# Kernel optimization log

Measured on AMD Instinct MI355X. Metric: run time of the kernel, lower is better.

Reference implementation:

```python
import jax, jax.numpy as jnp
import numpy as np

TAU_PLUS = 0.02
TAU_MINUS = 0.02
TAU_X = 0.101
A_TRIPLET = 0.0065
HOMEOSTATIC_RATE = 0.1
DT = 0.001
SPIKE_P = 0.05  # spike probability used to binarize inputs


def setup_inputs() -> dict:
    key = jax.random.key(0)
    k1, k2, k3 = jax.random.split(key, 3)
    B, P, Q, T = 16, 2048, 2048, 256
    pre_spikes = (jax.random.uniform(k1, (B, P, T)) < SPIKE_P).astype(jnp.float32)
    post_spikes = (jax.random.uniform(k2, (B, Q, T)) < SPIKE_P).astype(jnp.float32)
    weights = jax.random.normal(k3, (P, Q), dtype=jnp.float32) * 0.1
    meta_A_plus = jnp.float32(0.01)
    meta_A_minus = jnp.float32(0.012)
    return {"pre_spikes": pre_spikes, "post_spikes": post_spikes,
            "weights": weights, "meta_A_plus": meta_A_plus,
            "meta_A_minus": meta_A_minus}


def _traces(spikes_tbn, decay):
    """Trace value used at step t: x_t = decay * (x_{t-1} + s_{t-1}), x_0 = 0."""
    def step(carry, s):
        x = decay * carry          # decayed trace, used for this step's update
        return x + s, x            # spike added AFTER the update, per original
    init = jnp.zeros(spikes_tbn.shape[1:], spikes_tbn.dtype)
    _, xs = jax.lax.scan(step, init, spikes_tbn)
    return xs  # [T, B, N]


def reference(pre_spikes, post_spikes, weights, meta_A_plus, meta_A_minus):
    B, P, T = pre_spikes.shape
    exp_plus = jnp.exp(jnp.float32(-DT / TAU_PLUS))
    exp_minus = jnp.exp(jnp.float32(-DT / TAU_MINUS))
    exp_x = jnp.exp(jnp.float32(-DT / TAU_X))

    pre_t = jnp.transpose(pre_spikes, (2, 0, 1))    # [T, B, P]
    post_t = jnp.transpose(post_spikes, (2, 0, 1))  # [T, B, Q]

    x_pre = _traces(pre_t, exp_plus)     # [T, B, P]
    x_post = _traces(post_t, exp_minus)  # [T, B, Q]
    x_trip = _traces(post_t, exp_x)      # [T, B, Q]

    # Per-step outer products summed over time == one big contraction over (t, b).
    ltp = jnp.einsum('tbp,tbq->pq', x_pre, post_t) * meta_A_plus
    triplet = jnp.einsum('tbp,tbq->pq', x_pre, post_t * x_trip) * A_TRIPLET
    ltd = jnp.einsum('tbp,tbq->pq', pre_t, x_post) * meta_A_minus
    weight_updates = ltp + triplet - ltd

    # Homeostatic scaling (fresh module: activity history holds only this sample)
    current_activity = (pre_spikes.sum() + post_spikes.sum()) / (B * T)
    scaling_factor = jnp.sqrt(HOMEOSTATIC_RATE / (current_activity + 1e-6))

    updated_weights = weights + weight_updates * scaling_factor
    return jnp.clip(updated_weights, -2.0, 2.0)
```

## Files before the change

kernel.cpp:

```cpp
#include <hip/hip_runtime.h>


constexpr int TB = 16;
constexpr int NP = 2048;
constexpr int NQ = 2048;
constexpr int TT = 256;
constexpr int KH = TB * TT;
constexpr int KT = 2 * KH;

typedef unsigned short ushort_t;
typedef __attribute__((ext_vector_type(8))) __bf16 bf16x8;
typedef __attribute__((ext_vector_type(4))) float f32x4;

__device__ __forceinline__ unsigned bf1(float f) {
    unsigned u = __builtin_bit_cast(unsigned, f);
    return (u + 0x7FFFu + ((u >> 16) & 1u)) >> 16;
}
__device__ __forceinline__ unsigned pack2(float lo, float hi) {
    return bf1(lo) | (bf1(hi) << 16);
}
__device__ __forceinline__ unsigned spk2(float a, float b) {
    return ((a != 0.f) ? 0x3F80u : 0u) | ((b != 0.f) ? 0x3F800000u : 0u);
}

constexpr float DF1 = 0.95122942450071400910f;
constexpr float DF2 = DF1 * DF1;
constexpr float DF4 = DF2 * DF2;
constexpr float DF8 = DF4 * DF4;
constexpr float DF16 = DF8 * DF8;
constexpr float DF32 = DF16 * DF16;
constexpr float DF64 = DF32 * DF32;

constexpr float DX1 = 0.99014786386058731819f;
constexpr float DX2 = DX1 * DX1;
constexpr float DX4 = DX2 * DX2;
constexpr float DX8 = DX4 * DX4;
constexpr float DX16 = DX8 * DX8;
constexpr float DX32 = DX16 * DX16;
constexpr float DX64 = DX32 * DX32;

template <int K>
__device__ __forceinline__ float seg_step(float b, float pw, int sl) {
    float t = __shfl_up(b, K, 64);
    return (sl >= K) ? fmaf(pw, t, b) : b;
}
__device__ __forceinline__ float scan16(float c, float p1, float p2, float p4,
                                        float p8, int sl) {
    c = seg_step<1>(c, p1, sl);
    c = seg_step<2>(c, p2, sl);
    c = seg_step<4>(c, p4, sl);
    c = seg_step<8>(c, p8, sl);
    return c;
}
__device__ __forceinline__ float fold4(float4 u, float d) {
    float C = d * u.x;
    C = d * (C + u.y); C = d * (C + u.z); C = d * (C + u.w);
    return C;
}
__device__ __forceinline__ float4 expand4(float x, float4 u, float d) {
    float4 t;
    t.x = x; x = d * (x + u.x);
    t.y = x; x = d * (x + u.y);
    t.z = x; x = d * (x + u.z);
    t.w = x;
    return t;
}

__global__ __launch_bounds__(256) void stage_traces(
    const float* __restrict__ pre, const float* __restrict__ post,
    const float* __restrict__ mApP, const float* __restrict__ mAmP,
    ushort_t* __restrict__ Ab, ushort_t* __restrict__ Bb,
    float* __restrict__ partials)
{
    const int tid  = threadIdx.x;
    const int lane = tid & 63;
    const int wv   = tid >> 6;
    const int sl   = lane & 15;
    const int rowg = blockIdx.x * 16 + wv * 4 + (lane >> 4);
    const bool isPre = rowg < TB * NP;
    const int m = isPre ? rowg : rowg - TB * NP;
    const int b = m >> 11;
    const int r = m & 2047;

    const float4* srcRow = (const float4*)((isPre ? pre : post) + (size_t)m * TT);
    const float4 u0 = srcRow[sl];
    const float4 u1 = srcRow[16 + sl];
    const float4 u2 = srcRow[32 + sl];
    const float4 u3 = srcRow[48 + sl];

    float cnt = ((u0.x + u0.y) + (u0.z + u0.w)) + ((u1.x + u1.y) + (u1.z + u1.w))
              + ((u2.x + u2.y) + (u2.z + u2.w)) + ((u3.x + u3.y) + (u3.z + u3.w));

    const int hi = lane | 15;

    float bf0 = scan16(fold4(u0, DF1), DF4, DF8, DF16, DF32, sl);
    float bf1_ = scan16(fold4(u1, DF1), DF4, DF8, DF16, DF32, sl);
    float bf2 = scan16(fold4(u2, DF1), DF4, DF8, DF16, DF32, sl);
    float bf3 = scan16(fold4(u3, DF1), DF4, DF8, DF16, DF32, sl);
    const float Tf0 = __shfl(bf0, hi, 64);
    const float Tf1 = __shfl(bf1_, hi, 64);
    const float Tf2 = __shfl(bf2, hi, 64);
    const float Xf1 = Tf0;
    const float Xf2 = fmaf(DF64, Xf1, Tf1);
    const float Xf3 = fmaf(DF64, Xf2, Tf2);
    float ef0 = __shfl_up(bf0, 1, 64);
    float ef1 = __shfl_up(bf1_, 1, 64);
    float ef2 = __shfl_up(bf2, 1, 64);
    float ef3 = __shfl_up(bf3, 1, 64);
    if (sl == 0) { ef0 = 0.f; ef1 = 0.f; ef2 = 0.f; ef3 = 0.f; }
    float pf = 1.f;
    if (sl & 1) pf *= DF4;
    if (sl & 2) pf *= DF8;
    if (sl & 4) pf *= DF16;
    if (sl & 8) pf *= DF32;
    const float4 t0 = expand4(ef0,                 u0, DF1);
    const float4 t1 = expand4(fmaf(pf, Xf1, ef1),  u1, DF1);
    const float4 t2 = expand4(fmaf(pf, Xf2, ef2),  u2, DF1);
    const float4 t3 = expand4(fmaf(pf, Xf3, ef3),  u3, DF1);

    ushort_t* oA = (isPre ? Ab : Bb) + (size_t)r * KT + b * TT + 4 * sl;

    if (isPre) {
        *(uint2*)(oA)            = uint2{pack2(t0.x, t0.y), pack2(t0.z, t0.w)};
        *(uint2*)(oA + 64)       = uint2{pack2(t1.x, t1.y), pack2(t1.z, t1.w)};
        *(uint2*)(oA + 128)      = uint2{pack2(t2.x, t2.y), pack2(t2.z, t2.w)};
        *(uint2*)(oA + 192)      = uint2{pack2(t3.x, t3.y), pack2(t3.z, t3.w)};
        *(uint2*)(oA + KH)       = uint2{spk2(u0.x, u0.y), spk2(u0.z, u0.w)};
        *(uint2*)(oA + KH + 64)  = uint2{spk2(u1.x, u1.y), spk2(u1.z, u1.w)};
        *(uint2*)(oA + KH + 128) = uint2{spk2(u2.x, u2.y), spk2(u2.z, u2.w)};
        *(uint2*)(oA + KH + 192) = uint2{spk2(u3.x, u3.y), spk2(u3.z, u3.w)};
    } else {
        float bx0 = scan16(fold4(u0, DX1), DX4, DX8, DX16, DX32, sl);
        float bx1 = scan16(fold4(u1, DX1), DX4, DX8, DX16, DX32, sl);
        float bx2 = scan16(fold4(u2, DX1), DX4, DX8, DX16, DX32, sl);
        float bx3 = scan16(fold4(u3, DX1), DX4, DX8, DX16, DX32, sl);
        const float Tx0 = __shfl(bx0, hi, 64);
        const float Tx1 = __shfl(bx1, hi, 64);
        const float Tx2 = __shfl(bx2, hi, 64);
        const float Xx1 = Tx0;
        const float Xx2 = fmaf(DX64, Xx1, Tx1);
        const float Xx3 = fmaf(DX64, Xx2, Tx2);
        float ex0 = __shfl_up(bx0, 1, 64);
        float ex1 = __shfl_up(bx1, 1, 64);
        float ex2 = __shfl_up(bx2, 1, 64);
        float ex3 = __shfl_up(bx3, 1, 64);
        if (sl == 0) { ex0 = 0.f; ex1 = 0.f; ex2 = 0.f; ex3 = 0.f; }
        float px = 1.f;
        if (sl & 1) px *= DX4;
        if (sl & 2) px *= DX8;
        if (sl & 4) px *= DX16;
        if (sl & 8) px *= DX32;
        const float4 w0 = expand4(ex0,                u0, DX1);
        const float4 w1 = expand4(fmaf(px, Xx1, ex1), u1, DX1);
        const float4 w2 = expand4(fmaf(px, Xx2, ex2), u2, DX1);
        const float4 w3 = expand4(fmaf(px, Xx3, ex3), u3, DX1);

        const float Ap = *mApP;
        const float Am = *mAmP;
        auto av2 = [&](float sa, float ta, float sb, float tb) -> unsigned {
            unsigned lo = (sa != 0.f) ? bf1(fmaf(0.0065f, ta, Ap)) : 0u;
            unsigned hi2 = (sb != 0.f) ? bf1(fmaf(0.0065f, tb, Ap)) : 0u;
            return lo | (hi2 << 16);
        };
        *(uint2*)(oA)       = uint2{av2(u0.x, w0.x, u0.y, w0.y), av2(u0.z, w0.z, u0.w, w0.w)};
        *(uint2*)(oA + 64)  = uint2{av2(u1.x, w1.x, u1.y, w1.y), av2(u1.z, w1.z, u1.w, w1.w)};
        *(uint2*)(oA + 128) = uint2{av2(u2.x, w2.x, u2.y, w2.y), av2(u2.z, w2.z, u2.w, w2.w)};
        *(uint2*)(oA + 192) = uint2{av2(u3.x, w3.x, u3.y, w3.y), av2(u3.z, w3.z, u3.w, w3.w)};
        *(uint2*)(oA + KH)       = uint2{pack2(-Am * t0.x, -Am * t0.y), pack2(-Am * t0.z, -Am * t0.w)};
        *(uint2*)(oA + KH + 64)  = uint2{pack2(-Am * t1.x, -Am * t1.y), pack2(-Am * t1.z, -Am * t1.w)};
        *(uint2*)(oA + KH + 128) = uint2{pack2(-Am * t2.x, -Am * t2.y), pack2(-Am * t2.z, -Am * t2.w)};
        *(uint2*)(oA + KH + 192) = uint2{pack2(-Am * t3.x, -Am * t3.y), pack2(-Am * t3.z, -Am * t3.w)};
    }

    #pragma unroll
    for (int off = 32; off > 0; off >>= 1)
        cnt += __shfl_down(cnt, off, 64);
    __shared__ float wsum[4];
    if (lane == 0) wsum[wv] = cnt;
    __syncthreads();
    if (tid == 0)
        partials[blockIdx.x] = (wsum[0] + wsum[1]) + (wsum[2] + wsum[3]);
}

__device__ __forceinline__ void async16(const ushort_t* g, ushort_t* l) {
    __builtin_amdgcn_global_load_lds(
        (const __attribute__((address_space(1))) unsigned int*)g,
        (__attribute__((address_space(3))) unsigned int*)l,
        16, 0, 0);
}

#define FENCE() asm volatile("" ::: "memory")
#define BAR()   do { FENCE(); __builtin_amdgcn_s_barrier(); FENCE(); } while (0)
#define LGKM0() asm volatile("s_waitcnt lgkmcnt(0)" ::: "memory")
#define VMC8()  asm volatile("s_waitcnt vmcnt(8)" ::: "memory")
#define VMC0()  asm volatile("s_waitcnt vmcnt(0)" ::: "memory")

#define STAGE(GP, LP, KI, H) do {                                           \
    const ushort_t* _g = (GP) + (size_t)(H) * 128 * KT + (size_t)(KI) * 64; \
    ushort_t* _l = (LP) + (H) * 8192;                                       \
    async16(_g + ofG,  _l + ld0);                                           \
    async16(_g + ofG2, _l + ld1);                                           \
} while (0)

#define RD_A(BUF, QM) do {                                                  \
    _Pragma("unroll")                                                       \
    for (int mi = 0; mi < 4; ++mi) {                                        \
        const ushort_t* _r = &As[BUF][(QM) * 8192 + aBase + mi * 1024];     \
        af[mi][0] = *(const bf16x8*)(_r + sK0);                             \
        af[mi][1] = *(const bf16x8*)(_r + sK1);                             \
    }                                                                       \
} while (0)

#define RD_B(BUF, QN, BV) do {                                              \
    _Pragma("unroll")                                                       \
    for (int ni = 0; ni < 2; ++ni) {                                        \
        const ushort_t* _r = &Bs[BUF][(QN) * 8192 + bBase + ni * 1024];     \
        BV[ni][0] = *(const bf16x8*)(_r + sK0);                             \
        BV[ni][1] = *(const bf16x8*)(_r + sK1);                             \
    }                                                                       \
} while (0)

#define MFMAQ(QM, QN, BV) do {                                              \
    __builtin_amdgcn_s_setprio(1);                                          \
    _Pragma("unroll")                                                       \
    for (int ks = 0; ks < 2; ++ks)                                          \
        _Pragma("unroll")                                                   \
        for (int mi = 0; mi < 4; ++mi)                                      \
            _Pragma("unroll")                                               \
            for (int ni = 0; ni < 2; ++ni)                                  \
                acc[(QM)*4+mi][(QN)*2+ni] =                                 \
                    __builtin_amdgcn_mfma_f32_16x16x32_bf16(                \
                        af[mi][ks], BV[ni][ks],                             \
                        acc[(QM)*4+mi][(QN)*2+ni], 0, 0, 0);                \
    __builtin_amdgcn_s_setprio(0);                                          \
} while (0)

__global__ __launch_bounds__(512) void gemm8(
    const ushort_t* __restrict__ Ab, const ushort_t* __restrict__ Bb,
    const float* __restrict__ sp, float* __restrict__ scaleBuf,
    float* __restrict__ P0, float* __restrict__ P1,
    float* __restrict__ P2, float* __restrict__ P3)
{
    __shared__ ushort_t As[2][256 * 64];
    __shared__ ushort_t Bs[2][256 * 64];
    __shared__ float red[8];

    const int tid  = threadIdx.x;
    const int lane = tid & 63;
    const int wv   = tid >> 6;
    const int wr   = wv >> 2;
    const int wc   = wv & 3;
    const int quad = lane >> 4;
    const int m16  = lane & 15;

    if (blockIdx.x == 0) {
        float v = 0.f;
        #pragma unroll
        for (int i = 0; i < 8; ++i) v += sp[tid + i * 512];
        #pragma unroll
        for (int off = 32; off > 0; off >>= 1)
            v += __shfl_down(v, off, 64);
        if (lane == 0) red[wv] = v;
        __syncthreads();
        if (tid == 0) {
            float s = ((red[0] + red[1]) + (red[2] + red[3]))
                    + ((red[4] + red[5]) + (red[6] + red[7]));
            scaleBuf[0] = sqrtf(0.1f / (s * (1.0f / 4096.0f) + 1e-6f));
        }
    }

    const int id  = blockIdx.x;
    const int xcd = id & 7;
    const int j   = id >> 3;
    const int z   = j & 3;
    const int t   = j >> 2;
    const int pt  = ((xcd >> 1) << 1) | (t >> 2);
    const int qt  = ((xcd & 1) << 2) | (t & 3);
    const int p0  = pt * 256;
    const int q0  = qt * 256;
    const int kbase = z * (KT / 4);

    const ushort_t* Agp = Ab + (size_t)p0 * KT + kbase;
    const ushort_t* Bgp = Bb + (size_t)q0 * KT + kbase;
    const int rIn  = tid >> 3;
    const int rIn2 = rIn + 64;
    const size_t ofG  = (size_t)rIn  * KT + (size_t)((((tid & 7) ^ (rIn  & 7))) * 8);
    const size_t ofG2 = (size_t)rIn2 * KT + (size_t)((((tid & 7) ^ (rIn2 & 7))) * 8);
    const int ld0 = tid * 8;
    const int ld1 = 4096 + tid * 8;

    const int x8  = (m16 & 7) * 8;
    const int sK0 = (quad * 8) ^ x8;
    const int sK1 = ((quad + 4) * 8) ^ x8;
    const int aBase = (wr * 64 + m16) * 64;
    const int bBase = (wc * 32 + m16) * 64;

    f32x4 acc[8][4] = {};
    bf16x8 af[4][2], bv0[2][2], bv1[2][2];

    STAGE(Agp, As[0], 0, 0);
    STAGE(Agp, As[0], 0, 1);
    STAGE(Bgp, Bs[0], 0, 0);
    STAGE(Bgp, Bs[0], 0, 1);
    STAGE(Agp, As[1], 1, 0);
    STAGE(Agp, As[1], 1, 1);
    STAGE(Bgp, Bs[1], 1, 0);
    STAGE(Bgp, Bs[1], 1, 1);
    VMC8();
    BAR();

    #pragma unroll 1
    for (int it = 0; it < 16; ++it) {
        const int k2 = 2 * it;
        const bool pf = (it < 15);
        RD_A(0, 0);
        RD_B(0, 0, bv0);
        BAR(); LGKM0();
        MFMAQ(0, 0, bv0);
        BAR();
        RD_B(0, 1, bv1);
        if (pf) { STAGE(Agp, As[0], k2 + 2, 0); STAGE(Bgp, Bs[0], k2 + 2, 0); }
        BAR(); LGKM0();
        MFMAQ(0, 1, bv1);
        BAR();
        RD_A(0, 1);
        if (pf) STAGE(Bgp, Bs[0], k2 + 2, 1);
        BAR(); LGKM0();
        MFMAQ(1, 1, bv1);
        BAR();
        if (pf) STAGE(Agp, As[0], k2 + 2, 1);
        BAR();
        MFMAQ(1, 0, bv0);
        if (pf) { VMC8(); } else { VMC0(); }
        BAR();
        RD_A(1, 0);
        RD_B(1, 0, bv0);
        BAR(); LGKM0();
        MFMAQ(0, 0, bv0);
        BAR();
        RD_B(1, 1, bv1);
        if (pf) { STAGE(Agp, As[1], k2 + 3, 0); STAGE(Bgp, Bs[1], k2 + 3, 0); }
        BAR(); LGKM0();
        MFMAQ(0, 1, bv1);
        BAR();
        RD_A(1, 1);
        if (pf) STAGE(Bgp, Bs[1], k2 + 3, 1);
        BAR(); LGKM0();
        MFMAQ(1, 1, bv1);
        BAR();
        if (pf) STAGE(Agp, As[1], k2 + 3, 1);
        BAR();
        MFMAQ(1, 0, bv0);
        if (pf) { VMC8(); }
        BAR();
    }

    float* P = (z == 0) ? P0 : ((z == 1) ? P1 : ((z == 2) ? P2 : P3));
    #pragma unroll
    for (int m = 0; m < 8; ++m) {
        const int prow = p0 + ((m >> 2) << 7) + wr * 64 + (m & 3) * 16 + quad * 4;
        #pragma unroll
        for (int n = 0; n < 4; ++n) {
            const int qcol = q0 + ((n >> 1) << 7) + wc * 32 + (n & 1) * 16 + m16;
            #pragma unroll
            for (int r = 0; r < 4; ++r)
                P[(size_t)(prow + r) * NQ + qcol] = acc[m][n][r];
        }
    }
}

__global__ __launch_bounds__(256, 2) void gemm_split(
    const ushort_t* __restrict__ Ab, const ushort_t* __restrict__ Bb,
    const float* __restrict__ sp, float* __restrict__ scaleBuf,
    float* __restrict__ P0, float* __restrict__ P1)
{
    __shared__ ushort_t Ls[2][128 * 64];
    __shared__ ushort_t Rs[2][128 * 64];
    __shared__ float red[4];

    const int tid  = threadIdx.x;
    const int lane = tid & 63;
    const int wv   = tid >> 6;
    const int wr   = wv >> 1;
    const int wc   = wv & 1;
    const int quad = lane >> 4;
    const int m16  = lane & 15;

    if (blockIdx.x == 0) {
        float v = 0.f;
        #pragma unroll
        for (int i = 0; i < 16; ++i) v += sp[tid + i * 256];
        #pragma unroll
        for (int off = 32; off > 0; off >>= 1)
            v += __shfl_down(v, off, 64);
        if (lane == 0) red[wv] = v;
        __syncthreads();
        if (tid == 0) {
            float s = (red[0] + red[1]) + (red[2] + red[3]);
            scaleBuf[0] = sqrtf(0.1f / (s * (1.0f / 4096.0f) + 1e-6f));
        }
    }

    const int id  = blockIdx.x;
    const int xcd = id & 7;
    const int j5  = id >> 3;
    const int z   = j5 & 1;
    const int t   = j5 >> 1;
    const int pt  = ((xcd >> 1) << 2) + (t >> 3);
    const int qt  = ((xcd & 1) << 3) + (t & 7);

    const int p0 = pt * 128;
    const int q0 = qt * 128;
    const int kbase = z * (KT / 2);
    const int ldsbase = wv * 512;

    const ushort_t* gaP[4];
    const ushort_t* gbP[4];
    #pragma unroll
    for (int rr = 0; rr < 4; ++rr) {
        const int c   = rr * 256 + tid;
        const int row = c >> 3;
        const int kk8 = (c & 7) ^ (row & 7);
        gaP[rr] = Ab + (size_t)(p0 + row) * KT + kbase + kk8 * 8;
        gbP[rr] = Bb + (size_t)(q0 + row) * KT + kbase + kk8 * 8;
    }

    f32x4 acc[4][4] = {};

    auto stageF = [&](int buf) {
        #pragma unroll
        for (int rr = 0; rr < 4; ++rr) {
            async16(gaP[rr], &Ls[buf][rr * 2048 + ldsbase]);
            async16(gbP[rr], &Rs[buf][rr * 2048 + ldsbase]);
            gaP[rr] += 64;
            gbP[rr] += 64;
        }
    };
    auto computeF = [&](int buf) {
        #pragma unroll
        for (int ks = 0; ks < 2; ++ks) {
            bf16x8 afl[4], bfr[4];
            #pragma unroll
            for (int i = 0; i < 4; ++i) {
                const int row  = wr * 64 + i * 16 + m16;
                const int slot = (ks * 4 + quad) ^ (row & 7);
                afl[i] = *(const bf16x8*)&Ls[buf][row * 64 + slot * 8];
            }
            #pragma unroll
            for (int jj = 0; jj < 4; ++jj) {
                const int row  = wc * 64 + jj * 16 + m16;
                const int slot = (ks * 4 + quad) ^ (row & 7);
                bfr[jj] = *(const bf16x8*)&Rs[buf][row * 64 + slot * 8];
            }
            #pragma unroll
            for (int i = 0; i < 4; ++i)
                #pragma unroll
                for (int jj = 0; jj < 4; ++jj)
                    acc[i][jj] = __builtin_amdgcn_mfma_f32_16x16x32_bf16(
                        afl[i], bfr[jj], acc[i][jj], 0, 0, 0);
        }
    };

    constexpr int NIT = (KT / 2) / 64;
    stageF(0);
    for (int kt2 = 0; kt2 < NIT / 2; ++kt2) {
        __syncthreads();
        stageF(1);
        computeF(0);
        __syncthreads();
        if (kt2 + 1 < NIT / 2)
            stageF(0);
        computeF(1);
    }

    float* P = z ? P1 : P0;
    #pragma unroll
    for (int i = 0; i < 4; ++i) {
        const int prow = p0 + wr * 64 + i * 16 + quad * 4;
        #pragma unroll
        for (int jj = 0; jj < 4; ++jj) {
            const int qcol = q0 + wc * 64 + jj * 16 + m16;
            #pragma unroll
            for (int r2 = 0; r2 < 4; ++r2)
                P[(size_t)(prow + r2) * NQ + qcol] = acc[i][jj][r2];
        }
    }
}

__global__ __launch_bounds__(256) void merge_out4(
    const float* __restrict__ W, const float* __restrict__ P1,
    const float* __restrict__ P2, const float* __restrict__ P3,
    const float* __restrict__ scaleBuf, float* __restrict__ Out)
{
    const float scale = scaleBuf[0];
    const size_t i4 = (size_t)blockIdx.x * 256 + threadIdx.x;
    float4 w = ((const float4*)W)[i4];
    float4 a = ((const float4*)Out)[i4];
    float4 b = ((const float4*)P1)[i4];
    float4 c = ((const float4*)P2)[i4];
    float4 d = ((const float4*)P3)[i4];
    float4 o;
    o.x = fminf(fmaxf(fmaf(scale, (a.x + b.x) + (c.x + d.x), w.x), -2.f), 2.f);
    o.y = fminf(fmaxf(fmaf(scale, (a.y + b.y) + (c.y + d.y), w.y), -2.f), 2.f);
    o.z = fminf(fmaxf(fmaf(scale, (a.z + b.z) + (c.z + d.z), w.z), -2.f), 2.f);
    o.w = fminf(fmaxf(fmaf(scale, (a.w + b.w) + (c.w + d.w), w.w), -2.f), 2.f);
    ((float4*)Out)[i4] = o;
}

__global__ __launch_bounds__(256) void merge_out2(
    const float* __restrict__ W, const float* __restrict__ P1,
    const float* __restrict__ scaleBuf, float* __restrict__ Out)
{
    const float scale = scaleBuf[0];
    const size_t i4 = (size_t)blockIdx.x * 256 + threadIdx.x;
    float4 w = ((const float4*)W)[i4];
    float4 a = ((const float4*)Out)[i4];
    float4 c = ((const float4*)P1)[i4];
    float4 o;
    o.x = fminf(fmaxf(fmaf(scale, a.x + c.x, w.x), -2.f), 2.f);
    o.y = fminf(fmaxf(fmaf(scale, a.y + c.y, w.y), -2.f), 2.f);
    o.z = fminf(fmaxf(fmaf(scale, a.z + c.z, w.z), -2.f), 2.f);
    o.w = fminf(fmaxf(fmaf(scale, a.w + c.w, w.w), -2.f), 2.f);
    ((float4*)Out)[i4] = o;
}

extern "C" void kernel_launch(void* const* d_in, const int* in_sizes, int n_in,
                              void* d_out, int out_size, void* d_ws, size_t ws_size,
                              hipStream_t stream) {
    const float* pre  = (const float*)d_in[0];
    const float* post = (const float*)d_in[1];
    const float* W    = (const float*)d_in[2];
    const float* mAp  = (const float*)d_in[3];
    const float* mAm  = (const float*)d_in[4];
    float* out = (float*)d_out;

    const size_t AB = (size_t)NP * KT * 2;
    const size_t PB = (size_t)NP * NQ * 4;

    char* ws = (char*)d_ws;
    float* partials = (float*)ws;
    float* scaleBuf = (float*)(ws + 16384);
    ushort_t* Ab = (ushort_t*)(ws + 32768);
    ushort_t* Bb = (ushort_t*)(ws + 32768 + AB);
    float* P1 = (float*)(ws + 32768 + 2 * AB);
    float* P2 = (float*)(ws + 32768 + 2 * AB + PB);
    float* P3 = (float*)(ws + 32768 + 2 * AB + 2 * PB);

    stage_traces<<<dim3((TB * NP + TB * NQ) / 16), dim3(256), 0, stream>>>(
        pre, post, mAp, mAm, Ab, Bb, partials);

    if (ws_size >= 32768 + 2 * AB + 3 * PB) {
        gemm8<<<dim3(256), dim3(512), 0, stream>>>(
            Ab, Bb, partials, scaleBuf, out, P1, P2, P3);
        merge_out4<<<dim3(NP * NQ / 1024), dim3(256), 0, stream>>>(
            W, P1, P2, P3, scaleBuf, out);
    } else {
        gemm_split<<<dim3(512), dim3(256), 0, stream>>>(
            Ab, Bb, partials, scaleBuf, out, P1);
        merge_out2<<<dim3(NP * NQ / 1024), dim3(256), 0, stream>>>(
            W, P1, scaleBuf, out);
    }
}
```

Measured before the change: 200.1 us.

## Fuse split-K reduction and epilogue into GEMM via last-arriver atomic ticket

Removes the separate merge_out4 kernel by having each GEMM block take an atomic ticket per output tile after writing its split-K partial. The fourth block to finish reads the other three partials, computes the homeostatic scale itself from the stage partials, and writes the clipped final weights. This saves a kernel launch and one full pass over the output buffers, but the merge now runs on only a quarter of the blocks at the tail of the GEMM. The ticket counters are reset inside stage_traces, and the scalar reduction is repeated in every finishing block.

```diff
diff --git a/kernel.cpp b/kernel.cpp
--- a/kernel.cpp
+++ b/kernel.cpp
@@ -70,9 +70,11 @@
     const float* __restrict__ pre, const float* __restrict__ post,
     const float* __restrict__ mApP, const float* __restrict__ mAmP,
     ushort_t* __restrict__ Ab, ushort_t* __restrict__ Bb,
-    float* __restrict__ partials)
+    float* __restrict__ partials, int* __restrict__ cnt)
 {
     const int tid  = threadIdx.x;
+    if (blockIdx.x == 0 && tid < 64) cnt[tid] = 0;
+
     const int lane = tid & 63;
     const int wv   = tid >> 6;
     const int sl   = lane & 15;
@@ -88,8 +90,8 @@
     const float4 u2 = srcRow[32 + sl];
     const float4 u3 = srcRow[48 + sl];
 
-    float cnt = ((u0.x + u0.y) + (u0.z + u0.w)) + ((u1.x + u1.y) + (u1.z + u1.w))
-              + ((u2.x + u2.y) + (u2.z + u2.w)) + ((u3.x + u3.y) + (u3.z + u3.w));
+    float cnt_s = ((u0.x + u0.y) + (u0.z + u0.w)) + ((u1.x + u1.y) + (u1.z + u1.w))
+                + ((u2.x + u2.y) + (u2.z + u2.w)) + ((u3.x + u3.y) + (u3.z + u3.w));
 
     const int hi = lane | 15;
 
@@ -174,9 +176,9 @@
 
     #pragma unroll
     for (int off = 32; off > 0; off >>= 1)
-        cnt += __shfl_down(cnt, off, 64);
+        cnt_s += __shfl_down(cnt_s, off, 64);
     __shared__ float wsum[4];
-    if (lane == 0) wsum[wv] = cnt;
+    if (lane == 0) wsum[wv] = cnt_s;
     __syncthreads();
     if (tid == 0)
         partials[blockIdx.x] = (wsum[0] + wsum[1]) + (wsum[2] + wsum[3]);
@@ -235,15 +237,17 @@
     __builtin_amdgcn_s_setprio(0);                                          \
 } while (0)
 
-__global__ __launch_bounds__(512) void gemm8(
+__global__ __launch_bounds__(512) void gemm8f(
     const ushort_t* __restrict__ Ab, const ushort_t* __restrict__ Bb,
-    const float* __restrict__ sp, float* __restrict__ scaleBuf,
-    float* __restrict__ P0, float* __restrict__ P1,
-    float* __restrict__ P2, float* __restrict__ P3)
+    const float* __restrict__ sp, const float* __restrict__ W,
+    float* __restrict__ P0out, float* __restrict__ P1,
+    float* __restrict__ P2, float* __restrict__ P3,
+    int* __restrict__ cnt)
 {
     __shared__ ushort_t As[2][256 * 64];
     __shared__ ushort_t Bs[2][256 * 64];
     __shared__ float red[8];
+    __shared__ int ticket_s;
 
     const int tid  = threadIdx.x;
     const int lane = tid & 63;
@@ -252,22 +256,6 @@
     const int wc   = wv & 3;
     const int quad = lane >> 4;
     const int m16  = lane & 15;
-
-    if (blockIdx.x == 0) {
-        float v = 0.f;
-        #pragma unroll
-        for (int i = 0; i < 8; ++i) v += sp[tid + i * 512];
-        #pragma unroll
-        for (int off = 32; off > 0; off >>= 1)
-            v += __shfl_down(v, off, 64);
-        if (lane == 0) red[wv] = v;
-        __syncthreads();
-        if (tid == 0) {
-            float s = ((red[0] + red[1]) + (red[2] + red[3]))
-                    + ((red[4] + red[5]) + (red[6] + red[7]));
-            scaleBuf[0] = sqrtf(0.1f / (s * (1.0f / 4096.0f) + 1e-6f));
-        }
-    }
 
     const int id  = blockIdx.x;
     const int xcd = id & 7;
@@ -355,7 +343,7 @@
         BAR();
     }
 
-    float* P = (z == 0) ? P0 : ((z == 1) ? P1 : ((z == 2) ? P2 : P3));
+    float* P = (z == 0) ? P0out : ((z == 1) ? P1 : ((z == 2) ? P2 : P3));
     #pragma unroll
     for (int m = 0; m < 8; ++m) {
         const int prow = p0 + ((m >> 2) << 7) + wr * 64 + (m & 3) * 16 + quad * 4;
@@ -365,6 +353,44 @@
             #pragma unroll
             for (int r = 0; r < 4; ++r)
                 P[(size_t)(prow + r) * NQ + qcol] = acc[m][n][r];
+        }
+    }
+    __threadfence();
+    if (tid == 0) ticket_s = atomicAdd(&cnt[pt * 8 + qt], 1);
+    __syncthreads();
+    if (ticket_s != 3) return;
+    __threadfence();
+
+    float v = 0.f;
+    #pragma unroll
+    for (int i = 0; i < 8; ++i) v += sp[tid + i * 512];
+    #pragma unroll
+    for (int off = 32; off > 0; off >>= 1)
+        v += __shfl_down(v, off, 64);
+    if (lane == 0) red[wv] = v;
+    __syncthreads();
+    const float s = ((red[0] + red[1]) + (red[2] + red[3]))
+                  + ((red[4] + red[5]) + (red[6] + red[7]));
+    const float scale = sqrtf(0.1f / (s * (1.0f / 4096.0f) + 1e-6f));
+
+    const float* Pa; const float* Pb; const float* Pc;
+    if (z == 0)      { Pa = P1;    Pb = P2; Pc = P3; }
+    else if (z == 1) { Pa = P0out; Pb = P2; Pc = P3; }
+    else if (z == 2) { Pa = P0out; Pb = P1; Pc = P3; }
+    else             { Pa = P0out; Pb = P1; Pc = P2; }
+
+    #pragma unroll
+    for (int m = 0; m < 8; ++m) {
+        const int prow = p0 + ((m >> 2) << 7) + wr * 64 + (m & 3) * 16 + quad * 4;
+        #pragma unroll
+        for (int n = 0; n < 4; ++n) {
+            const int qcol = q0 + ((n >> 1) << 7) + wc * 32 + (n & 1) * 16 + m16;
+            #pragma unroll
+            for (int r = 0; r < 4; ++r) {
+                const size_t idx = (size_t)(prow + r) * NQ + qcol;
+                const float sum = acc[m][n][r] + ((Pa[idx] + Pb[idx]) + Pc[idx]);
+                P0out[idx] = fminf(fmaxf(fmaf(scale, sum, W[idx]), -2.f), 2.f);
+            }
         }
     }
 }
@@ -487,26 +513,6 @@
     }
 }
 
-__global__ __launch_bounds__(256) void merge_out4(
-    const float* __restrict__ W, const float* __restrict__ P1,
-    const float* __restrict__ P2, const float* __restrict__ P3,
-    const float* __restrict__ scaleBuf, float* __restrict__ Out)
-{
-    const float scale = scaleBuf[0];
-    const size_t i4 = (size_t)blockIdx.x * 256 + threadIdx.x;
-    float4 w = ((const float4*)W)[i4];
-    float4 a = ((const float4*)Out)[i4];
-    float4 b = ((const float4*)P1)[i4];
-    float4 c = ((const float4*)P2)[i4];
-    float4 d = ((const float4*)P3)[i4];
-    float4 o;
-    o.x = fminf(fmaxf(fmaf(scale, (a.x + b.x) + (c.x + d.x), w.x), -2.f), 2.f);
-    o.y = fminf(fmaxf(fmaf(scale, (a.y + b.y) + (c.y + d.y), w.y), -2.f), 2.f);
-    o.z = fminf(fmaxf(fmaf(scale, (a.z + b.z) + (c.z + d.z), w.z), -2.f), 2.f);
-    o.w = fminf(fmaxf(fmaf(scale, (a.w + b.w) + (c.w + d.w), w.w), -2.f), 2.f);
-    ((float4*)Out)[i4] = o;
-}
-
 __global__ __launch_bounds__(256) void merge_out2(
     const float* __restrict__ W, const float* __restrict__ P1,
     const float* __restrict__ scaleBuf, float* __restrict__ Out)
@@ -540,6 +546,7 @@
     char* ws = (char*)d_ws;
     float* partials = (float*)ws;
     float* scaleBuf = (float*)(ws + 16384);
+    int*   cnt      = (int*)(ws + 20480);
     ushort_t* Ab = (ushort_t*)(ws + 32768);
     ushort_t* Bb = (ushort_t*)(ws + 32768 + AB);
     float* P1 = (float*)(ws + 32768 + 2 * AB);
@@ -547,13 +554,11 @@
     float* P3 = (float*)(ws + 32768 + 2 * AB + 2 * PB);
 
     stage_traces<<<dim3((TB * NP + TB * NQ) / 16), dim3(256), 0, stream>>>(
-        pre, post, mAp, mAm, Ab, Bb, partials);
+        pre, post, mAp, mAm, Ab, Bb, partials, cnt);
 
     if (ws_size >= 32768 + 2 * AB + 3 * PB) {
-        gemm8<<<dim3(256), dim3(512), 0, stream>>>(
-            Ab, Bb, partials, scaleBuf, out, P1, P2, P3);
-        merge_out4<<<dim3(NP * NQ / 1024), dim3(256), 0, stream>>>(
-            W, P1, P2, P3, scaleBuf, out);
+        gemm8f<<<dim3(256), dim3(512), 0, stream>>>(
+            Ab, Bb, partials, W, out, P1, P2, P3, cnt);
     } else {
         gemm_split<<<dim3(512), dim3(256), 0, stream>>>(
             Ab, Bb, partials, scaleBuf, out, P1);
```

Result: slower. 310.1 us (+55.0%).
